# Kernel tuning notes

Measured on AMD Instinct MI355X. Metric: run time of the kernel, lower is better.

Reference implementation:

```python
import jax, jax.numpy as jnp
import numpy as np

B, N, D, H, T = 32, 4096, 256, 8, 28  # batch, nodes, hidden_dim, bottleneck_dim, horizon


def setup_inputs() -> dict:
    key = jax.random.key(0)
    ks = jax.random.split(key, 16)
    s = 0.1
    return {
        "x": jax.random.normal(ks[0], (B, N, D), jnp.float32),
        "last_step": jax.random.normal(ks[1], (B, N), jnp.float32),
        # GRU params (PyTorch layout: gates ordered r, z, n)
        "W_ih": jax.random.normal(ks[2], (3 * H, 1), jnp.float32) * s,
        "W_hh": jax.random.normal(ks[3], (3 * H, H), jnp.float32) * s,
        "b_ih": jax.random.normal(ks[4], (3 * H,), jnp.float32) * s,
        "b_hh": jax.random.normal(ks[5], (3 * H,), jnp.float32) * s,
        # hidden_proj: Linear(D -> H)
        "Wp": jax.random.normal(ks[6], (H, D), jnp.float32) * s,
        "bp": jax.random.normal(ks[7], (H,), jnp.float32) * s,
        # output_proj: Linear(H -> 1)
        "Wo": jax.random.normal(ks[8], (1, H), jnp.float32) * s,
        "bo": jax.random.normal(ks[9], (1,), jnp.float32) * s,
        # refine_gate: Linear(D->H), ReLU, Linear(H->T), Sigmoid
        "Wg1": jax.random.normal(ks[10], (H, D), jnp.float32) * s,
        "bg1": jax.random.normal(ks[11], (H,), jnp.float32) * s,
        "Wg2": jax.random.normal(ks[12], (T, H), jnp.float32) * s,
        "bg2": jax.random.normal(ks[13], (T,), jnp.float32) * s,
        "log_decay": jnp.float32(-2.3),
    }


def _rollout(x, last_step, W_ih, W_hh, b_ih, b_hh, Wp, bp, Wo, bo, Wg1, bg1, Wg2, bg2, log_decay):
    b, n, d = x.shape
    h = x.reshape(b * n, d) @ Wp.T + bp                 # [BN, H] initial GRU hidden
    cur = last_step.reshape(b * n)                       # scalar input per row
    w_ih = W_ih[:, 0]                                    # [3H] (input_size == 1)

    def step(carry, _):
        h, cur = carry
        gi = cur[:, None] * w_ih[None, :] + b_ih         # [BN, 3H]
        gh = h @ W_hh.T + b_hh                           # [BN, 3H]
        r = jax.nn.sigmoid(gi[:, :H] + gh[:, :H])
        z = jax.nn.sigmoid(gi[:, H:2 * H] + gh[:, H:2 * H])
        ncand = jnp.tanh(gi[:, 2 * H:] + r * gh[:, 2 * H:])
        h_new = (1.0 - z) * ncand + z * h
        pred = h_new @ Wo[0] + bo[0]                     # [BN]
        return (h_new, pred), pred

    (_, _), preds = jax.lax.scan(step, (h, cur), None, length=T)  # [T, BN]
    gru_pred = preds.T.reshape(b, n, T)                  # [B, N, T]

    gate = jax.nn.sigmoid(
        jax.nn.relu(jnp.einsum('bnd,hd->bnh', x, Wg1) + bg1) @ Wg2.T + bg2
    )                                                    # [B, N, T]
    time_steps = jnp.arange(1, T + 1, dtype=x.dtype)
    decay_curve = jnp.exp(-jnp.exp(log_decay) * time_steps)       # [T]
    decay_pred = last_step[..., None] * decay_curve               # [B, N, T]
    return gate * gru_pred + (1.0 - gate) * decay_pred


def reference(x, last_step, W_ih, W_hh, b_ih, b_hh, Wp, bp, Wo, bo, Wg1, bg1, Wg2, bg2, log_decay):
    return _rollout(x, last_step, W_ih, W_hh, b_ih, b_hh, Wp, bp, Wo, bo, Wg1, bg1, Wg2, bg2, log_decay)
```

## Files before the change

kernel.cpp:

```cpp
#include <hip/hip_runtime.h>

#define TT 28
#define L2E 1.4426950408889634f

typedef __attribute__((ext_vector_type(8))) short bf16x8;
typedef __attribute__((ext_vector_type(4))) float f32x4;
typedef _Float16 h2 __attribute__((ext_vector_type(2)));
typedef __fp16 fp16x2 __attribute__((ext_vector_type(2)));

__device__ __forceinline__ unsigned fbits(float f){ union{float f; unsigned u;} v; v.f=f; return v.u; }
__device__ __forceinline__ float bitsf(unsigned u){ union{unsigned u; float f;} v; v.u=u; return v.f; }
__device__ __forceinline__ short bf16rnd(float f){ return (short)((fbits(f)+0x8000u)>>16); }

__device__ __forceinline__ h2 PKH2(float a, float b){
    fp16x2 t = __builtin_amdgcn_cvt_pkrtz(a, b);
    return __builtin_bit_cast(h2, t);
}

#if __has_builtin(__builtin_amdgcn_fdot2)
#define FDOT2(a,b,c) __builtin_amdgcn_fdot2((a),(b),(c),false)
#else
__device__ __forceinline__ float FDOT2(h2 a, h2 b, float c){
    return fmaf((float)a.x,(float)b.x, fmaf((float)a.y,(float)b.y,(c)));
}
#endif
#if __has_builtin(__builtin_amdgcn_exp2f)
#define EXP2(x) __builtin_amdgcn_exp2f(x)
#else
#define EXP2(x) exp2f(x)
#endif
#if __has_builtin(__builtin_amdgcn_rcpf)
#define RCP(x) __builtin_amdgcn_rcpf(x)
#else
#define RCP(x) (1.f/(x))
#endif

__global__ __launch_bounds__(256) __attribute__((amdgpu_waves_per_eu(2, 2)))
void horizon_kernel(
    const float* __restrict__ x, const float* __restrict__ last_step,
    const float* __restrict__ W_ih, const float* __restrict__ W_hh,
    const float* __restrict__ b_ih, const float* __restrict__ b_hh,
    const float* __restrict__ Wp, const float* __restrict__ bp,
    const float* __restrict__ Wo, const float* __restrict__ bo,
    const float* __restrict__ Wg1, const float* __restrict__ bg1,
    const float* __restrict__ Wg2, const float* __restrict__ bg2,
    const float* __restrict__ log_decay, float* __restrict__ out)
{
    __shared__ __attribute__((aligned(16))) float s_whh[24*8];
    __shared__ __attribute__((aligned(16))) float s_gate[28][12];
    __shared__ __attribute__((aligned(16))) float s_wiabc[32];
    __shared__ __attribute__((aligned(16))) float s_wb4[32];
    __shared__ __attribute__((aligned(16))) float s_dyn[4][64*29];

    const int tid = threadIdx.x;

    if (tid < 192) s_whh[tid] = W_hh[tid] * (tid < 128 ? L2E : 2.0f*L2E);
    if (tid < 224) s_gate[tid>>3][tid&7] = Wg2[tid] * L2E;
    if (tid < 28)  s_gate[tid][8] = bg2[tid] * L2E;
    if (tid < 16){ s_wiabc[2*tid] = W_ih[tid]*L2E; s_wiabc[2*tid+1] = (b_ih[tid] + b_hh[tid])*L2E; }
    if (tid < 8){
        s_wb4[4*tid+0] = W_ih[16+tid]*2.0f*L2E;
        s_wb4[4*tid+1] = b_ih[16+tid]*2.0f*L2E;
        s_wb4[4*tid+2] = b_hh[16+tid]*2.0f*L2E;
        s_wb4[4*tid+3] = Wo[tid];
    }
    __syncthreads();

    const int lane = tid & 63;
    const int wv   = tid >> 6;
    const int c    = lane >> 4;
    const int rl   = lane & 15;
    const int group = blockIdx.x*4 + wv;
    float* dyn = &s_dyn[wv][0];

    const float* wrow = (rl < 8) ? (Wp + rl*256) : (Wg1 + (rl-8)*256);
    bf16x8 bfrag[8];
    #pragma unroll
    for (int kk=0; kk<8; ++kk){
        #pragma unroll
        for (int j=0; j<8; ++j) bfrag[kk][j] = bf16rnd(wrow[kk*32 + c*8 + j]);
    }
    const float aBias = (rl < 8) ? bp[rl] : bg1[rl-8];

    #pragma unroll 2
    for (int sub=0; sub<4; ++sub){
        const float* xrow = x + (size_t)(group*64 + sub*16 + rl) * 256;
        f32x4 acc = {0.f, 0.f, 0.f, 0.f};
        #pragma unroll
        for (int kk=0; kk<8; ++kk){
            float4 v0 = *(const float4*)(xrow + kk*32 + c*8);
            float4 v1 = *(const float4*)(xrow + kk*32 + c*8 + 4);
            float xs[8] = {v0.x,v0.y,v0.z,v0.w, v1.x,v1.y,v1.z,v1.w};
            bf16x8 ahi, alo;
            #pragma unroll
            for (int j=0; j<8; ++j){
                unsigned u  = fbits(xs[j]);
                unsigned hb = (u + 0x8000u) & 0xFFFF0000u;
                ahi[j] = (short)(hb >> 16);
                alo[j] = bf16rnd(xs[j] - bitsf(hb));
            }
            acc = __builtin_amdgcn_mfma_f32_16x16x32_bf16(ahi, bfrag[kk], acc, 0, 0, 0);
            acc = __builtin_amdgcn_mfma_f32_16x16x32_bf16(alo, bfrag[kk], acc, 0, 0, 0);
        }
        #pragma unroll
        for (int r=0; r<4; ++r){
            float v = acc[r] + aBias;
            if (rl >= 8) v = fmaxf(v, 0.f);
            dyn[(sub*16 + c*4 + r)*20 + rl] = v;
        }
    }

    float h[8], q[8];
    #pragma unroll
    for (int j=0; j<8; ++j){ h[j] = dyn[lane*20 + j]; q[j] = dyn[lane*20 + 8 + j]; }

    float w1[16], bb1[16];
    #pragma unroll
    for (int p=0; p<8; ++p){
        float4 wb = *(const float4*)&s_wiabc[p*4];
        w1[2*p] = wb.x; bb1[2*p] = wb.y; w1[2*p+1] = wb.z; bb1[2*p+1] = wb.w;
    }
    float w2[8], bi2[8], bh2c[8], wo8[8];
    #pragma unroll
    for (int j=0; j<8; ++j){
        float4 wb = *(const float4*)&s_wb4[4*j];
        w2[j] = wb.x; bi2[j] = wb.y; bh2c[j] = wb.z; wo8[j] = wb.w;
    }
    h2 whh2[24][4];
    #pragma unroll
    for (int o=0; o<24; ++o){
        float4 wa = *(const float4*)&s_whh[o*8];
        float4 wc = *(const float4*)&s_whh[o*8+4];
        whh2[o][0] = PKH2(wa.x, wa.y); whh2[o][1] = PKH2(wa.z, wa.w);
        whh2[o][2] = PKH2(wc.x, wc.y); whh2[o][3] = PKH2(wc.z, wc.w);
    }

    const int lrow  = group*64 + lane;
    const float ls0 = last_step[lrow];
    float cur   = ls0;
    const float df = __expf(-__expf(log_decay[0]));
    float decay = 1.f;
    const float boS = bo[0];

    #pragma unroll 1
    for (int t=0; t<TT; ++t){
        h2 hh[4];
        #pragma unroll
        for (int k=0; k<4; ++k) hh[k] = PKH2(h[2*k], h[2*k+1]);

        float s[16];
        #pragma unroll
        for (int o=0; o<16; ++o){
            float a = fmaf(cur, w1[o], bb1[o]);
            #pragma unroll
            for (int k=0; k<4; ++k) a = FDOT2(hh[k], whh2[o][k], a);
            s[o] = a;
        }
        float nn[8], zz[8];
        #pragma unroll
        for (int o=0; o<8; ++o){
            float g = bh2c[o];
            #pragma unroll
            for (int k=0; k<4; ++k) g = FDOT2(hh[k], whh2[16+o][k], g);
            float r  = RCP(1.f + EXP2(-s[o]));
            float un = fmaf(r, g, fmaf(cur, w2[o], bi2[o]));
            float e2 = EXP2(un);
            nn[o] = fmaf(-2.f, RCP(e2 + 1.f), 1.f);
            zz[o] = RCP(1.f + EXP2(-s[8+o]));
        }
        float pred = boS;
        #pragma unroll
        for (int j=0; j<8; ++j){
            h[j] = fmaf(zz[j], h[j]-nn[j], nn[j]);
            pred = fmaf(h[j], wo8[j], pred);
        }
        float4 ga = *(const float4*)&s_gate[t][0];
        float4 gb = *(const float4*)&s_gate[t][4];
        float gl = s_gate[t][8];
        gl = fmaf(ga.x,q[0],gl); gl = fmaf(ga.y,q[1],gl); gl = fmaf(ga.z,q[2],gl); gl = fmaf(ga.w,q[3],gl);
        gl = fmaf(gb.x,q[4],gl); gl = fmaf(gb.y,q[5],gl); gl = fmaf(gb.z,q[6],gl); gl = fmaf(gb.w,q[7],gl);
        float gate = RCP(1.f + EXP2(-gl));

        decay *= df;
        float dp = ls0 * decay;
        dyn[lane*29 + t] = fmaf(gate, pred - dp, dp);
        cur = pred;
    }

    float o28[TT];
    #pragma unroll
    for (int t=0; t<TT; ++t) o28[t] = dyn[lane*29 + t];
    float* orow = out + (size_t)lrow * TT;
    #pragma unroll
    for (int i=0; i<7; ++i){
        float4 v = make_float4(o28[4*i], o28[4*i+1], o28[4*i+2], o28[4*i+3]);
        *(float4*)(orow + 4*i) = v;
    }
}

extern "C" void kernel_launch(void* const* d_in, const int* in_sizes, int n_in,
                              void* d_out, int out_size, void* d_ws, size_t ws_size,
                              hipStream_t stream)
{
    const float* x         = (const float*)d_in[0];
    const float* last_step = (const float*)d_in[1];
    const float* W_ih      = (const float*)d_in[2];
    const float* W_hh      = (const float*)d_in[3];
    const float* b_ih      = (const float*)d_in[4];
    const float* b_hh      = (const float*)d_in[5];
    const float* Wp        = (const float*)d_in[6];
    const float* bp        = (const float*)d_in[7];
    const float* Wo        = (const float*)d_in[8];
    const float* bo        = (const float*)d_in[9];
    const float* Wg1       = (const float*)d_in[10];
    const float* bg1       = (const float*)d_in[11];
    const float* Wg2       = (const float*)d_in[12];
    const float* bg2       = (const float*)d_in[13];
    const float* log_decay = (const float*)d_in[14];

    hipLaunchKernelGGL(horizon_kernel, dim3(512), dim3(256), 0, stream,
                       x, last_step, W_ih, W_hh, b_ih, b_hh, Wp, bp, Wo, bo,
                       Wg1, bg1, Wg2, bg2, log_decay, (float*)d_out);
}
```

Before: 258.5 us.

## Split each row's GRU recurrence across four lanes with DPP hidden-state exchange

Each block now handles 64 rows instead of 256, so the grid grows fourfold. Four threads cooperate on one row, each owning two hidden units and exchanging hidden values with DPP xor-1/xor-2 moves every step. The 28-step serial GRU chain per thread becomes shorter per step, and the gate and decay outputs are computed in parallel per lane instead of inside the loop. Occupancy hints are raised to 5-8 waves per EU to hide latency. The cost is extra cross-lane traffic per step and redundant FDOT2 work for the output projection on all four lanes.

```diff
diff --git a/kernel.cpp b/kernel.cpp
--- a/kernel.cpp
+++ b/kernel.cpp
@@ -35,7 +35,15 @@
 #define RCP(x) (1.f/(x))
 #endif
 
-__global__ __launch_bounds__(256) __attribute__((amdgpu_waves_per_eu(2, 2)))
+#if __has_builtin(__builtin_amdgcn_mov_dpp)
+#define DPP_XOR1(x) __builtin_bit_cast(float, __builtin_amdgcn_mov_dpp(__builtin_bit_cast(int,(float)(x)), 0xB1, 0xF, 0xF, true))
+#define DPP_XOR2(x) __builtin_bit_cast(float, __builtin_amdgcn_mov_dpp(__builtin_bit_cast(int,(float)(x)), 0x4E, 0xF, 0xF, true))
+#else
+#define DPP_XOR1(x) __shfl_xor((x), 1, 64)
+#define DPP_XOR2(x) __shfl_xor((x), 2, 64)
+#endif
+
+__global__ __launch_bounds__(256) __attribute__((amdgpu_waves_per_eu(5, 8)))
 void horizon_kernel(
     const float* __restrict__ x, const float* __restrict__ last_step,
     const float* __restrict__ W_ih, const float* __restrict__ W_hh,
@@ -47,22 +55,26 @@
     const float* __restrict__ log_decay, float* __restrict__ out)
 {
     __shared__ __attribute__((aligned(16))) float s_whh[24*8];
-    __shared__ __attribute__((aligned(16))) float s_gate[28][12];
-    __shared__ __attribute__((aligned(16))) float s_wiabc[32];
-    __shared__ __attribute__((aligned(16))) float s_wb4[32];
-    __shared__ __attribute__((aligned(16))) float s_dyn[4][64*29];
+    __shared__ __attribute__((aligned(16))) float s_wih[24];
+    __shared__ __attribute__((aligned(16))) float s_b1[16];
+    __shared__ __attribute__((aligned(16))) float s_bin[8];
+    __shared__ __attribute__((aligned(16))) float s_bhn[8];
+    __shared__ __attribute__((aligned(16))) float s_wo[8];
+    __shared__ __attribute__((aligned(16))) float s_gw[28*8];
+    __shared__ __attribute__((aligned(16))) float s_gb[28];
+    __shared__ __attribute__((aligned(16))) float s_park[64][17];
 
     const int tid = threadIdx.x;
 
     if (tid < 192) s_whh[tid] = W_hh[tid] * (tid < 128 ? L2E : 2.0f*L2E);
-    if (tid < 224) s_gate[tid>>3][tid&7] = Wg2[tid] * L2E;
-    if (tid < 28)  s_gate[tid][8] = bg2[tid] * L2E;
-    if (tid < 16){ s_wiabc[2*tid] = W_ih[tid]*L2E; s_wiabc[2*tid+1] = (b_ih[tid] + b_hh[tid])*L2E; }
+    if (tid < 224) s_gw[tid]  = Wg2[tid] * L2E;
+    if (tid < 28)  s_gb[tid]  = bg2[tid] * L2E;
+    if (tid < 24)  s_wih[tid] = W_ih[tid] * (tid < 16 ? L2E : 2.0f*L2E);
+    if (tid < 16)  s_b1[tid]  = (b_ih[tid] + b_hh[tid]) * L2E;
     if (tid < 8){
-        s_wb4[4*tid+0] = W_ih[16+tid]*2.0f*L2E;
-        s_wb4[4*tid+1] = b_ih[16+tid]*2.0f*L2E;
-        s_wb4[4*tid+2] = b_hh[16+tid]*2.0f*L2E;
-        s_wb4[4*tid+3] = Wo[tid];
+        s_bin[tid] = b_ih[16+tid] * (2.0f*L2E);
+        s_bhn[tid] = b_hh[16+tid] * (2.0f*L2E);
+        s_wo[tid]  = Wo[tid];
     }
     __syncthreads();
 
@@ -70,21 +82,18 @@
     const int wv   = tid >> 6;
     const int c    = lane >> 4;
     const int rl   = lane & 15;
-    const int group = blockIdx.x*4 + wv;
-    float* dyn = &s_dyn[wv][0];
-
-    const float* wrow = (rl < 8) ? (Wp + rl*256) : (Wg1 + (rl-8)*256);
-    bf16x8 bfrag[8];
-    #pragma unroll
-    for (int kk=0; kk<8; ++kk){
-        #pragma unroll
-        for (int j=0; j<8; ++j) bfrag[kk][j] = bf16rnd(wrow[kk*32 + c*8 + j]);
-    }
-    const float aBias = (rl < 8) ? bp[rl] : bg1[rl-8];
-
-    #pragma unroll 2
-    for (int sub=0; sub<4; ++sub){
-        const float* xrow = x + (size_t)(group*64 + sub*16 + rl) * 256;
+    const int rowBase = blockIdx.x * 64;
+
+    {
+        const float* wrow = (rl < 8) ? (Wp + rl*256) : (Wg1 + (rl-8)*256);
+        bf16x8 bfrag[8];
+        #pragma unroll
+        for (int kk=0; kk<8; ++kk){
+            #pragma unroll
+            for (int j=0; j<8; ++j) bfrag[kk][j] = bf16rnd(wrow[kk*32 + c*8 + j]);
+        }
+        const float aBias = (rl < 8) ? bp[rl] : bg1[rl-8];
+        const float* xrow = x + (size_t)(rowBase + wv*16 + rl) * 256;
         f32x4 acc = {0.f, 0.f, 0.f, 0.f};
         #pragma unroll
         for (int kk=0; kk<8; ++kk){
@@ -106,95 +115,103 @@
         for (int r=0; r<4; ++r){
             float v = acc[r] + aBias;
             if (rl >= 8) v = fmaxf(v, 0.f);
-            dyn[(sub*16 + c*4 + r)*20 + rl] = v;
-        }
-    }
-
-    float h[8], q[8];
-    #pragma unroll
-    for (int j=0; j<8; ++j){ h[j] = dyn[lane*20 + j]; q[j] = dyn[lane*20 + 8 + j]; }
-
-    float w1[16], bb1[16];
-    #pragma unroll
-    for (int p=0; p<8; ++p){
-        float4 wb = *(const float4*)&s_wiabc[p*4];
-        w1[2*p] = wb.x; bb1[2*p] = wb.y; w1[2*p+1] = wb.z; bb1[2*p+1] = wb.w;
-    }
-    float w2[8], bi2[8], bh2c[8], wo8[8];
-    #pragma unroll
-    for (int j=0; j<8; ++j){
-        float4 wb = *(const float4*)&s_wb4[4*j];
-        w2[j] = wb.x; bi2[j] = wb.y; bh2c[j] = wb.z; wo8[j] = wb.w;
-    }
-    h2 whh2[24][4];
-    #pragma unroll
-    for (int o=0; o<24; ++o){
-        float4 wa = *(const float4*)&s_whh[o*8];
-        float4 wc = *(const float4*)&s_whh[o*8+4];
-        whh2[o][0] = PKH2(wa.x, wa.y); whh2[o][1] = PKH2(wa.z, wa.w);
-        whh2[o][2] = PKH2(wc.x, wc.y); whh2[o][3] = PKH2(wc.z, wc.w);
-    }
-
-    const int lrow  = group*64 + lane;
-    const float ls0 = last_step[lrow];
-    float cur   = ls0;
-    const float df = __expf(-__expf(log_decay[0]));
-    float decay = 1.f;
+            s_park[wv*16 + c*4 + r][rl] = v;
+        }
+    }
+
+    const int row = tid >> 2;
+    const int o   = tid & 3;
+    const int rowG = rowBase + row;
+    const int dd0 = o, dd1 = o^1, dd2 = o^2, dd3 = o^3;
+
+    float harr[8];
+    harr[0]=s_park[row][dd0]; harr[1]=s_park[row][dd1]; harr[2]=s_park[row][dd2]; harr[3]=s_park[row][dd3];
+    harr[4]=s_park[row][4+dd0]; harr[5]=s_park[row][4+dd1]; harr[6]=s_park[row][4+dd2]; harr[7]=s_park[row][4+dd3];
+    float hOwn0 = harr[0], hOwn1 = harr[4];
+    h2 hh[4] = { PKH2(harr[0],harr[1]), PKH2(harr[2],harr[3]),
+                 PKH2(harr[4],harr[5]), PKH2(harr[6],harr[7]) };
+
+    const int rws[6] = { o, o+4, 8+o, 12+o, 16+o, 20+o };
+    h2 wk[6][4];
+    #pragma unroll
+    for (int rr=0; rr<6; ++rr){
+        const float* wp_ = &s_whh[rws[rr]*8];
+        wk[rr][0] = PKH2(wp_[dd0], wp_[dd1]); wk[rr][1] = PKH2(wp_[dd2], wp_[dd3]);
+        wk[rr][2] = PKH2(wp_[4+dd0], wp_[4+dd1]); wk[rr][3] = PKH2(wp_[4+dd2], wp_[4+dd3]);
+    }
+    const float w_r0 = s_wih[o],    w_r1 = s_wih[o+4];
+    const float w_z0 = s_wih[8+o],  w_z1 = s_wih[12+o];
+    const float w_n0 = s_wih[16+o], w_n1 = s_wih[20+o];
+    const float b_r0 = s_b1[o],   b_r1 = s_b1[o+4];
+    const float b_z0 = s_b1[8+o], b_z1 = s_b1[12+o];
+    const float b_in0 = s_bin[o], b_in1 = s_bin[o+4];
+    const float b_hn0 = s_bhn[o], b_hn1 = s_bhn[o+4];
+    h2 wo2[4] = { PKH2(s_wo[dd0], s_wo[dd1]), PKH2(s_wo[dd2], s_wo[dd3]),
+                  PKH2(s_wo[4+dd0], s_wo[4+dd1]), PKH2(s_wo[4+dd2], s_wo[4+dd3]) };
+
+    float qv[8];
+    #pragma unroll
+    for (int j=0; j<8; ++j) qv[j] = s_park[row][8+j];
+    float gates[7];
+    #pragma unroll
+    for (int i=0; i<7; ++i){
+        const int t = 4*i + o;
+        const float* gw = &s_gw[t*8];
+        float gl = s_gb[t];
+        #pragma unroll
+        for (int j=0; j<8; ++j) gl = fmaf(gw[j], qv[j], gl);
+        gates[i] = RCP(1.f + EXP2(-gl));
+    }
+
+    const float ls0 = last_step[rowG];
     const float boS = bo[0];
-
-    #pragma unroll 1
+    float cur = ls0;
+    float preds[7];
+
+    #pragma unroll
     for (int t=0; t<TT; ++t){
-        h2 hh[4];
-        #pragma unroll
-        for (int k=0; k<4; ++k) hh[k] = PKH2(h[2*k], h[2*k+1]);
-
-        float s[16];
-        #pragma unroll
-        for (int o=0; o<16; ++o){
-            float a = fmaf(cur, w1[o], bb1[o]);
-            #pragma unroll
-            for (int k=0; k<4; ++k) a = FDOT2(hh[k], whh2[o][k], a);
-            s[o] = a;
-        }
-        float nn[8], zz[8];
-        #pragma unroll
-        for (int o=0; o<8; ++o){
-            float g = bh2c[o];
-            #pragma unroll
-            for (int k=0; k<4; ++k) g = FDOT2(hh[k], whh2[16+o][k], g);
-            float r  = RCP(1.f + EXP2(-s[o]));
-            float un = fmaf(r, g, fmaf(cur, w2[o], bi2[o]));
-            float e2 = EXP2(un);
-            nn[o] = fmaf(-2.f, RCP(e2 + 1.f), 1.f);
-            zz[o] = RCP(1.f + EXP2(-s[8+o]));
-        }
-        float pred = boS;
-        #pragma unroll
-        for (int j=0; j<8; ++j){
-            h[j] = fmaf(zz[j], h[j]-nn[j], nn[j]);
-            pred = fmaf(h[j], wo8[j], pred);
-        }
-        float4 ga = *(const float4*)&s_gate[t][0];
-        float4 gb = *(const float4*)&s_gate[t][4];
-        float gl = s_gate[t][8];
-        gl = fmaf(ga.x,q[0],gl); gl = fmaf(ga.y,q[1],gl); gl = fmaf(ga.z,q[2],gl); gl = fmaf(ga.w,q[3],gl);
-        gl = fmaf(gb.x,q[4],gl); gl = fmaf(gb.y,q[5],gl); gl = fmaf(gb.z,q[6],gl); gl = fmaf(gb.w,q[7],gl);
-        float gate = RCP(1.f + EXP2(-gl));
-
-        decay *= df;
-        float dp = ls0 * decay;
-        dyn[lane*29 + t] = fmaf(gate, pred - dp, dp);
-        cur = pred;
-    }
-
-    float o28[TT];
-    #pragma unroll
-    for (int t=0; t<TT; ++t) o28[t] = dyn[lane*29 + t];
-    float* orow = out + (size_t)lrow * TT;
+        float sr0 = fmaf(cur, w_r0, b_r0), sr1 = fmaf(cur, w_r1, b_r1);
+        float sz0 = fmaf(cur, w_z0, b_z0), sz1 = fmaf(cur, w_z1, b_z1);
+        float gn0 = b_hn0, gn1 = b_hn1;
+        #pragma unroll
+        for (int k=0; k<4; ++k){
+            sr0 = FDOT2(hh[k], wk[0][k], sr0);
+            sr1 = FDOT2(hh[k], wk[1][k], sr1);
+            sz0 = FDOT2(hh[k], wk[2][k], sz0);
+            sz1 = FDOT2(hh[k], wk[3][k], sz1);
+            gn0 = FDOT2(hh[k], wk[4][k], gn0);
+            gn1 = FDOT2(hh[k], wk[5][k], gn1);
+        }
+        float r0 = RCP(1.f + EXP2(-sr0)), r1 = RCP(1.f + EXP2(-sr1));
+        float e0 = EXP2(fmaf(r0, gn0, fmaf(cur, w_n0, b_in0)));
+        float e1 = EXP2(fmaf(r1, gn1, fmaf(cur, w_n1, b_in1)));
+        float nn0 = fmaf(-2.f, RCP(e0 + 1.f), 1.f);
+        float nn1 = fmaf(-2.f, RCP(e1 + 1.f), 1.f);
+        float z0 = RCP(1.f + EXP2(-sz0)), z1 = RCP(1.f + EXP2(-sz1));
+        hOwn0 = fmaf(z0, hOwn0 - nn0, nn0);
+        hOwn1 = fmaf(z1, hOwn1 - nn1, nn1);
+
+        float a0 = DPP_XOR1(hOwn0), a1 = DPP_XOR1(hOwn1);
+        float u0 = DPP_XOR2(hOwn0), u1 = DPP_XOR2(a0);
+        float u2 = DPP_XOR2(hOwn1), u3 = DPP_XOR2(a1);
+        hh[0] = PKH2(hOwn0, a0); hh[1] = PKH2(u0, u1);
+        hh[2] = PKH2(hOwn1, a1); hh[3] = PKH2(u2, u3);
+
+        float p = boS;
+        #pragma unroll
+        for (int k=0; k<4; ++k) p = FDOT2(hh[k], wo2[k], p);
+        preds[t>>2] = ((t & 3) == o) ? p : preds[t>>2];
+        cur = p;
+    }
+
+    const float lam = EXP2(log_decay[0] * L2E);
+    const float c1  = -lam * L2E;
+    float* orow = out + (size_t)rowG * TT;
     #pragma unroll
     for (int i=0; i<7; ++i){
-        float4 v = make_float4(o28[4*i], o28[4*i+1], o28[4*i+2], o28[4*i+3]);
-        *(float4*)(orow + 4*i) = v;
+        const int t = 4*i + o;
+        float dp = ls0 * EXP2(c1 * (float)(t+1));
+        orow[t] = fmaf(gates[i], preds[i] - dp, dp);
     }
 }
 
@@ -218,7 +235,7 @@
     const float* bg2       = (const float*)d_in[13];
     const float* log_decay = (const float*)d_in[14];
 
-    hipLaunchKernelGGL(horizon_kernel, dim3(512), dim3(256), 0, stream,
+    hipLaunchKernelGGL(horizon_kernel, dim3(2048), dim3(256), 0, stream,
                        x, last_step, W_ih, W_hh, b_ih, b_hh, Wp, bp, Wo, bo,
                        Wg1, bg1, Wg2, bg2, log_decay, (float*)d_out);
 }
```

Result: faster. 234.2 us (-9.4%).
